# Kernel optimization log

Hardware: AMD Instinct MI355X
Metric: run time of the kernel (lower is better)

## Reference

```python
import jax, jax.numpy as jnp
import numpy as np

C = 768      # channel
H = 6        # height = 4 + 2*pre_step
W = 6        # width  = 4 + 2*pre_step
NB = 3       # n_block = H/2
SPLIT = 6    # = width
LS = 1536    # lstm_size = C * H / NB
NH = 4       # attention heads
DM = 512     # attention d_model
DK = DM // NH
B = 256


def setup_inputs() -> dict:
    key = jax.random.key(0)
    ks = jax.random.split(key, 20)
    s_l = 1.0 / np.sqrt(LS)
    s_a = 1.0 / np.sqrt(C)
    s_o = 1.0 / np.sqrt(DM)
    u = lambda k, shape, s: jax.random.uniform(k, shape, jnp.float32, -s, s)
    return {
        "x": jax.random.normal(ks[0], (B, H * W, C), jnp.float32),
        # 2-layer LSTM encoder (input=hidden=LS), torch gate order i,f,g,o
        "enc_Wih": u(ks[1], (2, 4 * LS, LS), s_l),
        "enc_Whh": u(ks[2], (2, 4 * LS, LS), s_l),
        "enc_bih": u(ks[3], (2, 4 * LS), s_l),
        "enc_bhh": u(ks[4], (2, 4 * LS), s_l),
        # 2-layer LSTM decoder
        "dec_Wih": u(ks[5], (2, 4 * LS, LS), s_l),
        "dec_Whh": u(ks[6], (2, 4 * LS, LS), s_l),
        "dec_bih": u(ks[7], (2, 4 * LS), s_l),
        "dec_bhh": u(ks[8], (2, 4 * LS), s_l),
        # multi-head attention: 768 -> 512 (4 heads x 128) -> 768
        "Wq": u(ks[9], (C, DM), s_a), "bq": u(ks[10], (DM,), s_a),
        "Wk": u(ks[11], (C, DM), s_a), "bk": u(ks[12], (DM,), s_a),
        "Wv": u(ks[13], (C, DM), s_a), "bv": u(ks[14], (DM,), s_a),
        "Wo": u(ks[15], (DM, C), s_o), "bo": u(ks[16], (C,), s_o),
        # LayerNorm over channel
        "ln_g": jnp.ones((C,), jnp.float32),
        "ln_b": jnp.zeros((C,), jnp.float32),
    }


def _cell(x, h, c, Wi, Wh, bi, bh):
    g = x @ Wi.T + bi + h @ Wh.T + bh
    i, f, gg, o = jnp.split(g, 4, axis=-1)
    c = jax.nn.sigmoid(f) * c + jax.nn.sigmoid(i) * jnp.tanh(gg)
    h = jax.nn.sigmoid(o) * jnp.tanh(c)
    return h, c


def _step2(st, xt, Wih, Whh, bih, bhh):
    # one timestep of a 2-layer LSTM
    h0, c0, h1, c1 = st
    h0, c0 = _cell(xt, h0, c0, Wih[0], Whh[0], bih[0], bhh[0])
    h1, c1 = _cell(h0, h1, c1, Wih[1], Whh[1], bih[1], bhh[1])
    return (h0, c0, h1, c1), h1


def _forward(x, enc_Wih, enc_Whh, enc_bih, enc_bhh,
             dec_Wih, dec_Whh, dec_bih, dec_bhh,
             Wq, bq, Wk, bk, Wv, bv, Wo, bo, ln_g, ln_b):
    Bx = x.shape[0]
    xb = x.reshape(Bx, NB, 2, W, C)
    # per block, each column j is a single-timestep feature concatenating the 2 rows
    # -> time-major sequence (SPLIT, NB*Bx, LS), blocks folded into the batch dim
    seq = jnp.transpose(xb, (3, 1, 0, 2, 4)).reshape(W, NB * Bx, LS)
    z = jnp.zeros((NB * Bx, LS), x.dtype)
    carry0 = (z, z, z, z)
    # encoder consumes columns in reversed order (j = split-1 .. 0)
    enc_st, enc_ys = jax.lax.scan(
        lambda s, xt: _step2(s, xt, enc_Wih, enc_Whh, enc_bih, enc_bhh),
        carry0, seq[::-1])
    en_out = enc_ys[-1]

    def dec_step(carry, _):
        st, inp = carry
        st, out = _step2(st, inp, dec_Wih, dec_Whh, dec_bih, dec_bhh)
        return (st, out), out
    _, dec_ys = jax.lax.scan(dec_step, (enc_st, en_out), None, length=SPLIT)

    # dec_ys: (SPLIT, NB*Bx, LS) -> xout_total: (NB, Bx, 2, SPLIT, C)
    xout = dec_ys.reshape(SPLIT, NB, Bx, 2, C).transpose(1, 2, 3, 0, 4)
    xt = xout.reshape(NB, Bx, 2 * SPLIT, C)

    # neighbor-block q/k, own-block v (NB=3): i=0 -> (q1,k2,v0); i=1 -> (q0,k2,v1); i=2 -> (q1,k0,v2)
    q = xt[jnp.array([1, 0, 1])]
    k = xt[jnp.array([2, 2, 0])]
    v = xt
    T = 2 * SPLIT
    Q = (q @ Wq + bq).reshape(NB, Bx, T, NH, DK)
    K = (k @ Wk + bk).reshape(NB, Bx, T, NH, DK)
    V = (v @ Wv + bv).reshape(NB, Bx, T, NH, DK)
    scores = jnp.einsum('nbqhd,nbkhd->nbhqk', Q, K) / np.float32(np.sqrt(DK))
    att = jax.nn.softmax(scores, axis=-1)
    o = jnp.einsum('nbhqk,nbkhd->nbqhd', att, V).reshape(NB, Bx, T, DM)
    o = o @ Wo + bo  # (NB, Bx, T, C)

    # concat blocks along height, layernorm over channel
    feat = o.reshape(NB, Bx, 2, W, C).transpose(1, 0, 2, 3, 4).reshape(Bx, H * W, C)
    mu = feat.mean(-1, keepdims=True)
    var = feat.var(-1, keepdims=True)
    feature = (feat - mu) / jnp.sqrt(var + 1e-5) * ln_g + ln_b
    out_decode = feature.reshape(Bx, H, W, C)[:, 1:5, 1:5, :]
    return feature, out_decode


def reference(x, enc_Wih, enc_Whh, enc_bih, enc_bhh,
              dec_Wih, dec_Whh, dec_bih, dec_bhh,
              Wq, bq, Wk, bk, Wv, bv, Wo, bo, ln_g, ln_b):
    return _forward(x, enc_Wih, enc_Whh, enc_bih, enc_bhh,
                    dec_Wih, dec_Whh, dec_bih, dec_bhh,
                    Wq, bq, Wk, bk, Wv, bv, Wo, bo, ln_g, ln_b)
```

## Files before the change

kernel.cpp:

```cpp
#include <hip/hip_runtime.h>


typedef unsigned short u16;
typedef unsigned int   u32;
typedef __bf16 bf16x8 __attribute__((ext_vector_type(8)));
typedef short  short8 __attribute__((ext_vector_type(8)));
typedef float  f32x4  __attribute__((ext_vector_type(4)));

__device__ __forceinline__ u16 f2bf(float f) {
  u32 u = __float_as_uint(f);
  u32 r = u + 0x7FFFu + ((u >> 16) & 1u);
  return (u16)(r >> 16);
}

__device__ __forceinline__ f32x4 mfma16(short8 a, short8 b, f32x4 c) {
  return __builtin_amdgcn_mfma_f32_16x16x32_bf16(
      __builtin_bit_cast(bf16x8, a), __builtin_bit_cast(bf16x8, b), c, 0, 0, 0);
}

__device__ __forceinline__ void gload16(const u16* g, u16* l) {
  __builtin_amdgcn_global_load_lds(
      (const __attribute__((address_space(1))) u32*)g,
      (__attribute__((address_space(3))) u32*)l, 16, 0, 0);
}

__global__ __launch_bounds__(256, 2) void lstm_cell(
    const u16* __restrict__ X, const u16* __restrict__ H,
    const u16* __restrict__ Wih, const u16* __restrict__ Whh,
    const float* __restrict__ bi, const float* __restrict__ bh,
    float* __restrict__ c, u16* __restrict__ hout, u16* __restrict__ h2)
{
  __shared__ __align__(16) u16 smem[32768];
  const int tid  = threadIdx.x;
  const int wid  = (blockIdx.x & 7) * 36 + (blockIdx.x >> 3);
  const int strip = wid / 6;
  const int bm    = wid - strip * 6;
  const int strip32 = strip * 32;
  const int lane = tid & 63, wave = tid >> 6;
  const int rh = wave & 1, hh = wave >> 1;
  const int r16  = lane & 15, kg = lane >> 4;
  const int srow = lane >> 2, sslot = lane & 3;

  f32x4 acc[4][4];
#pragma unroll
  for (int i = 0; i < 4; ++i)
#pragma unroll
    for (int j = 0; j < 4; ++j) acc[i][j] = (f32x4)0.0f;

  auto stage = [&](int i, int buf) {
    const u16* A = (i < 48) ? X : H;
    const u16* W = (i < 48) ? Wih : Whh;
    const int k0 = ((i < 48) ? i : (i - 48)) << 5;
#pragma unroll
    for (int cc2 = 0; cc2 < 2; ++cc2) {
      const int call = wave * 2 + cc2;
      const int row  = call * 16 + srow;
      const int slog = sslot ^ ((row >> 1) & 3);
      gload16(A + (size_t)(bm * 128 + row) * 1536 + k0 + slog * 8,
              smem + buf * 4096 + call * 512);
      const int g  = call >> 1;
      const int hr = (call & 1) * 16 + srow;
      gload16(W + ((size_t)g * 1536 + strip32 + hr) * 1536 + k0 + slog * 8,
              smem + 16384 + buf * 4096 + call * 512);
    }
  };

  auto computeFrom = [&](int i) {
    const u16* baseA = smem + (i & 3) * 4096;
    const u16* baseB = smem + 16384 + (i & 3) * 4096;
    short8 af[4], bfr[4];
#pragma unroll
    for (int mi = 0; mi < 4; ++mi) {
      const int row = rh * 64 + mi * 16 + r16;
      af[mi] = *(const short8*)(baseA + row * 32 + ((kg ^ ((row >> 1) & 3)) << 3));
    }
#pragma unroll
    for (int ni = 0; ni < 4; ++ni) {
      const int row = ni * 32 + hh * 16 + r16;
      bfr[ni] = *(const short8*)(baseB + row * 32 + ((kg ^ ((row >> 1) & 3)) << 3));
    }
#pragma unroll
    for (int mi = 0; mi < 4; ++mi)
#pragma unroll
      for (int ni = 0; ni < 4; ++ni)
        acc[mi][ni] = mfma16(af[mi], bfr[ni], acc[mi][ni]);
  };

  stage(0, 0); stage(1, 1); stage(2, 2); stage(3, 3);

  for (int i = 0; i < 93; ++i) {
    asm volatile("s_waitcnt vmcnt(12)" ::: "memory");
    __builtin_amdgcn_sched_barrier(0);
    __builtin_amdgcn_s_barrier();
    computeFrom(i);
    __builtin_amdgcn_s_barrier();
    __builtin_amdgcn_sched_barrier(0);
    if (i + 4 < 96) stage(i + 4, i & 3);
  }
  asm volatile("s_waitcnt vmcnt(8)" ::: "memory");
  __builtin_amdgcn_s_barrier();
  computeFrom(93);
  __builtin_amdgcn_s_barrier();
  asm volatile("s_waitcnt vmcnt(4)" ::: "memory");
  __builtin_amdgcn_s_barrier();
  computeFrom(94);
  __builtin_amdgcn_s_barrier();
  asm volatile("s_waitcnt vmcnt(0)" ::: "memory");
  __builtin_amdgcn_s_barrier();
  computeFrom(95);

  const int h = strip32 + hh * 16 + r16;
  float bsum[4];
#pragma unroll
  for (int ni = 0; ni < 4; ++ni)
    bsum[ni] = bi[ni * 1536 + h] + bh[ni * 1536 + h];
#pragma unroll
  for (int mi = 0; mi < 4; ++mi) {
    const int row0 = bm * 128 + rh * 64 + mi * 16 + kg * 4;
#pragma unroll
    for (int j = 0; j < 4; ++j) {
      const float ig = acc[mi][0][j] + bsum[0];
      const float fg = acc[mi][1][j] + bsum[1];
      const float gz = acc[mi][2][j] + bsum[2];
      const float og = acc[mi][3][j] + bsum[3];
      const float si = 1.0f / (1.0f + expf(-ig));
      const float sf = 1.0f / (1.0f + expf(-fg));
      const float so = 1.0f / (1.0f + expf(-og));
      const size_t cij = (size_t)(row0 + j) * 1536 + h;
      const float cnew = sf * c[cij] + si * tanhf(gz);
      c[cij] = cnew;
      const u16 hv = f2bf(so * tanhf(cnew));
      hout[cij] = hv;
      if (h2) h2[cij] = hv;
    }
  }
}

template <int OUT_BF16, int HAS_BIAS>
__global__ __launch_bounds__(256, 2) void gemm_bt(
    const u16* __restrict__ A1, const u16* __restrict__ B1, int K1,
    const float* __restrict__ bias, void* __restrict__ Cout, int N)
{
  __shared__ __align__(16) u16 smem[16384];
  const int tid  = threadIdx.x;
  const int bn   = blockIdx.x * 128;
  const int bm   = blockIdx.y * 128;
  const int lane = tid & 63, wave = tid >> 6;
  const int wm   = (wave >> 1) * 64, wn = (wave & 1) * 64;
  const int r16  = lane & 15, kg = lane >> 4;
  const int srow = lane >> 2, sslot = lane & 3;

  f32x4 acc[4][4];
#pragma unroll
  for (int i = 0; i < 4; ++i)
#pragma unroll
    for (int j = 0; j < 4; ++j) acc[i][j] = (f32x4)0.0f;

  const int nt = K1 >> 5;
  auto stage = [&](int i, int buf) {
    const int k0 = i << 5;
#pragma unroll
    for (int cc2 = 0; cc2 < 2; ++cc2) {
      const int call = wave * 2 + cc2;
      const int row  = call * 16 + srow;
      const int slog = sslot ^ ((row >> 1) & 3);
      gload16(A1 + (size_t)(bm + row) * K1 + k0 + slog * 8, smem + buf * 4096 + call * 512);
      gload16(B1 + (size_t)(bn + row) * K1 + k0 + slog * 8, smem + 8192 + buf * 4096 + call * 512);
    }
  };

  stage(0, 0);
  __syncthreads();
  int cur = 0;
  for (int i = 0; i < nt; ++i) {
    if (i + 1 < nt) stage(i + 1, cur ^ 1);
    const u16* baseA = smem + cur * 4096;
    const u16* baseB = smem + 8192 + cur * 4096;
    short8 af[4], bfr[4];
#pragma unroll
    for (int mi = 0; mi < 4; ++mi) {
      const int row = wm + mi * 16 + r16;
      af[mi] = *(const short8*)(baseA + row * 32 + ((kg ^ ((row >> 1) & 3)) << 3));
    }
#pragma unroll
    for (int ni = 0; ni < 4; ++ni) {
      const int row = wn + ni * 16 + r16;
      bfr[ni] = *(const short8*)(baseB + row * 32 + ((kg ^ ((row >> 1) & 3)) << 3));
    }
#pragma unroll
    for (int mi = 0; mi < 4; ++mi)
#pragma unroll
      for (int ni = 0; ni < 4; ++ni)
        acc[mi][ni] = mfma16(af[mi], bfr[ni], acc[mi][ni]);
    __syncthreads();
    cur ^= 1;
  }

  const size_t Ns = (size_t)N;
#pragma unroll
  for (int ni = 0; ni < 4; ++ni) {
    const int col = bn + wn + ni * 16 + r16;
    const float bvv = HAS_BIAS ? bias[col] : 0.0f;
#pragma unroll
    for (int mi = 0; mi < 4; ++mi) {
      const int row0 = bm + wm + mi * 16 + kg * 4;
      f32x4 v = acc[mi][ni];
#pragma unroll
      for (int j = 0; j < 4; ++j) {
        const float val = v[j] + bvv;
        const size_t idx = (size_t)(row0 + j) * Ns + col;
        if (OUT_BF16) ((u16*)Cout)[idx] = f2bf(val);
        else          ((float*)Cout)[idx] = val;
      }
    }
  }
}

__global__ __launch_bounds__(256) void attn_kernel(const u16* __restrict__ P, u16* __restrict__ O)
{
  __shared__ __align__(16) u16 sQ[12 * 520];
  __shared__ __align__(16) u16 sK[12 * 520];
  __shared__ __align__(16) u16 sVT[512 * 24];
  __shared__ __align__(16) u16 sS[4 * 16 * 16];
  const int tid = threadIdx.x;
  const int nb = blockIdx.x >> 8;
  const int b  = blockIdx.x & 255;
  const int qb = (nb == 1) ? 0 : 1;
  const int kb = (nb == 2) ? 0 : 2;
  const size_t rq = ((size_t)qb * 256 + b) * 12;
  const size_t rk = ((size_t)kb * 256 + b) * 12;
  const size_t rv = ((size_t)nb * 256 + b) * 12;

  for (int e4 = tid; e4 < 1536; e4 += 256) {
    const int t  = e4 >> 7;
    const int cc = (e4 & 127) * 4;
    uint2 qv = *(const uint2*)(P + (rq + t) * 1536 + cc);
    *(uint2*)(sQ + t * 520 + cc) = qv;
    uint2 kv = *(const uint2*)(P + (rk + t) * 1536 + 512 + cc);
    *(uint2*)(sK + t * 520 + cc) = kv;
    uint2 vv = *(const uint2*)(P + (rv + t) * 1536 + 1024 + cc);
    sVT[(cc + 0) * 24 + t] = (u16)(vv.x & 0xffff);
    sVT[(cc + 1) * 24 + t] = (u16)(vv.x >> 16);
    sVT[(cc + 2) * 24 + t] = (u16)(vv.y & 0xffff);
    sVT[(cc + 3) * 24 + t] = (u16)(vv.y >> 16);
  }
  for (int i = tid; i < 2048; i += 256) sVT[(i >> 2) * 24 + 12 + (i & 3)] = 0;
  __syncthreads();

  const int lane = tid & 63, h = tid >> 6;
  const int r16 = lane & 15, kg = lane >> 4;
  const int hcol = h * 128;

  f32x4 sc = (f32x4)0.0f;
#pragma unroll
  for (int ks = 0; ks < 4; ++ks) {
    short8 aq  = (r16 < 12) ? *(const short8*)(sQ + r16 * 520 + hcol + ks * 32 + kg * 8) : (short8)0;
    short8 bk2 = (r16 < 12) ? *(const short8*)(sK + r16 * 520 + hcol + ks * 32 + kg * 8) : (short8)0;
    sc = mfma16(aq, bk2, sc);
  }
  const float scale = 0.08838834764831845f;
#pragma unroll
  for (int j = 0; j < 4; ++j) {
    float v = (r16 < 12) ? sc[j] * scale : -1e30f;
    float m = v;
#pragma unroll
    for (int d = 1; d < 16; d <<= 1) m = fmaxf(m, __shfl_xor(m, d));
    float e = expf(v - m);
    float s = e;
#pragma unroll
    for (int d = 1; d < 16; d <<= 1) s += __shfl_xor(s, d);
    sS[h * 256 + (kg * 4 + j) * 16 + r16] = f2bf(e / s);
  }
  __syncthreads();
  short8 av = (kg < 2) ? *(const short8*)(sS + h * 256 + r16 * 16 + kg * 8) : (short8)0;
#pragma unroll
  for (int dt = 0; dt < 8; ++dt) {
    short8 bv2 = (kg < 2) ? *(const short8*)(sVT + (hcol + dt * 16 + r16) * 24 + kg * 8) : (short8)0;
    f32x4 ov = mfma16(av, bv2, (f32x4)0.0f);
    if (kg < 3) {
#pragma unroll
      for (int j = 0; j < 4; ++j) {
        const int q = kg * 4 + j;
        O[(rv + q) * 512 + hcol + dt * 16 + r16] = f2bf(ov[j]);
      }
    }
  }
}

__global__ __launch_bounds__(256) void layernorm_kernel(
    const float* __restrict__ feat, const float* __restrict__ gam,
    const float* __restrict__ bet, float* __restrict__ out)
{
  const int row = blockIdx.x;
  const int b = row / 36, hidx = row - b * 36;
  const int nb = hidx / 12, t = hidx - nb * 12;
  const float* src = feat + ((size_t)nb * 3072 + b * 12 + t) * 768;
  const int tid = threadIdx.x;
  float v0 = src[tid], v1 = src[tid + 256], v2 = src[tid + 512];
  float s = v0 + v1 + v2, sq = v0 * v0 + v1 * v1 + v2 * v2;
#pragma unroll
  for (int d = 1; d < 64; d <<= 1) { s += __shfl_xor(s, d); sq += __shfl_xor(sq, d); }
  __shared__ float ps[4], pq[4];
  if ((tid & 63) == 0) { ps[tid >> 6] = s; pq[tid >> 6] = sq; }
  __syncthreads();
  s  = ps[0] + ps[1] + ps[2] + ps[3];
  sq = pq[0] + pq[1] + pq[2] + pq[3];
  const float mean = s * (1.0f / 768.0f);
  const float var  = sq * (1.0f / 768.0f) - mean * mean;
  const float rstd = rsqrtf(var + 1e-5f);
  float* dst = out + (size_t)row * 768;
  const int hh = hidx / 6, wp = hidx - hh * 6;
  float* dst2 = nullptr;
  if (hh >= 1 && hh < 5 && wp >= 1 && wp < 5)
    dst2 = out + 7077888 + ((size_t)b * 16 + (hh - 1) * 4 + (wp - 1)) * 768;
#pragma unroll
  for (int i = 0; i < 3; ++i) {
    const int cix = tid + i * 256;
    const float vv = (i == 0) ? v0 : (i == 1 ? v1 : v2);
    const float o = (vv - mean) * rstd * gam[cix] + bet[cix];
    dst[cix] = o;
    if (dst2) dst2[cix] = o;
  }
}

__global__ __launch_bounds__(256) void cast_bf16_kernel(const float* __restrict__ src,
                                                        u16* __restrict__ dst, int n4)
{
  const int i = blockIdx.x * 256 + threadIdx.x;
  if (i >= n4) return;
  float4 v = ((const float4*)src)[i];
  uint2 pk;
  pk.x = (u32)f2bf(v.x) | ((u32)f2bf(v.y) << 16);
  pk.y = (u32)f2bf(v.z) | ((u32)f2bf(v.w) << 16);
  ((uint2*)dst)[i] = pk;
}

__global__ __launch_bounds__(256) void pack_qkvT(const float* __restrict__ Wq,
    const float* __restrict__ Wk, const float* __restrict__ Wv, u16* __restrict__ dst)
{
  const int idx = blockIdx.x * 256 + threadIdx.x;
  if (idx >= 1536 * 768) return;
  const int d = idx / 768, c = idx - d * 768;
  float v;
  if (d < 512)       v = Wq[(size_t)c * 512 + d];
  else if (d < 1024) v = Wk[(size_t)c * 512 + d - 512];
  else               v = Wv[(size_t)c * 512 + d - 1024];
  dst[idx] = f2bf(v);
}

__global__ __launch_bounds__(256) void pack_bias(const float* __restrict__ bq,
    const float* __restrict__ bk, const float* __restrict__ bv, float* __restrict__ dst)
{
  const int i = blockIdx.x * 256 + threadIdx.x;
  if (i < 512)       dst[i] = bq[i];
  else if (i < 1024) dst[i] = bk[i - 512];
  else if (i < 1536) dst[i] = bv[i - 1024];
}

__global__ __launch_bounds__(256) void pack_WoT(const float* __restrict__ Wo, u16* __restrict__ dst)
{
  const int idx = blockIdx.x * 256 + threadIdx.x;
  if (idx >= 768 * 512) return;
  const int n = idx / 512, k = idx - n * 512;
  dst[idx] = f2bf(Wo[(size_t)k * 768 + n]);
}

__global__ __launch_bounds__(256) void build_Xe(const float* __restrict__ x, u16* __restrict__ Xe)
{
  const int i4 = blockIdx.x * 256 + threadIdx.x;
  if (i4 >= 1769472) return;
  const int e = i4 * 4;
  const int c = e % 768;
  const int r2 = (e / 768) & 1;
  const int r = (e / 1536) % 768;
  const int s = e / 1179648;
  const int nb = r >> 8, bb = r & 255;
  const int w = 5 - s;
  const float* src = x + ((size_t)bb * 36 + (nb * 2 + r2) * 6 + w) * 768 + c;
  float4 v = *(const float4*)src;
  uint2 pk;
  pk.x = (u32)f2bf(v.x) | ((u32)f2bf(v.y) << 16);
  pk.y = (u32)f2bf(v.z) | ((u32)f2bf(v.w) << 16);
  ((uint2*)Xe)[i4] = pk;
}

__global__ __launch_bounds__(256) void build_xt(const u16* __restrict__ decys, u16* __restrict__ xt)
{
  const int i4 = blockIdx.x * 256 + threadIdx.x;
  if (i4 >= 1769472) return;
  const int e = i4 * 4;
  const int c = e % 768;
  const int t = (e / 768) % 12;
  const int b = (e / 9216) % 256;
  const int nb = e / 2359296;
  const int r2 = t / 6, s = t - r2 * 6;
  const u16* src = decys + ((size_t)s * 768 + nb * 256 + b) * 1536 + r2 * 768 + c;
  ((uint2*)xt)[i4] = *(const uint2*)src;
}

extern "C" void kernel_launch(void* const* d_in, const int* in_sizes, int n_in,
                              void* d_out, int out_size, void* d_ws, size_t ws_size,
                              hipStream_t stream)
{
  const float* x    = (const float*)d_in[0];
  const float* eWih = (const float*)d_in[1];
  const float* eWhh = (const float*)d_in[2];
  const float* ebih = (const float*)d_in[3];
  const float* ebhh = (const float*)d_in[4];
  const float* dWih = (const float*)d_in[5];
  const float* dWhh = (const float*)d_in[6];
  const float* dbih = (const float*)d_in[7];
  const float* dbhh = (const float*)d_in[8];
  const float* Wq = (const float*)d_in[9];
  const float* bq = (const float*)d_in[10];
  const float* Wk = (const float*)d_in[11];
  const float* bk = (const float*)d_in[12];
  const float* Wv = (const float*)d_in[13];
  const float* bv = (const float*)d_in[14];
  const float* Wo = (const float*)d_in[15];
  const float* bo = (const float*)d_in[16];
  const float* lng = (const float*)d_in[17];
  const float* lnb = (const float*)d_in[18];

  char* ws = (char*)d_ws;
  const size_t WBYTES = 37748736;
  u16* Weih = (u16*)(ws);
  u16* Wehh = (u16*)(ws + WBYTES);
  u16* Wdih = (u16*)(ws + 2 * WBYTES);
  u16* Wdhh = (u16*)(ws + 3 * WBYTES);
  u16*   xtb   = (u16*)(ws);
  u16*   Pqkv  = (u16*)(ws + 14155776);
  u16*   Obuf  = (u16*)(ws + 14155776 + 28311552);
  float* feato = (float*)(ws + 14155776 + 28311552 + 9437184);
  size_t off = 4 * WBYTES;
  auto take = [&](size_t bytes) -> char* {
    char* p = ws + off;
    off = (off + bytes + 255) & ~(size_t)255;
    return p;
  };
  u16* Wqkv  = (u16*)take((size_t)1536 * 768 * 2);
  float* bqkv = (float*)take(1536 * 4);
  u16* WoT   = (u16*)take((size_t)768 * 512 * 2);
  u16* Xe    = (u16*)take((size_t)6 * 768 * 1536 * 2);
  u16* h0a   = (u16*)take((size_t)768 * 1536 * 2);
  u16* h0b   = (u16*)take((size_t)768 * 1536 * 2);
  u16* h1a   = (u16*)take((size_t)768 * 1536 * 2);
  u16* h1b   = (u16*)take((size_t)768 * 1536 * 2);
  float* c0  = (float*)take((size_t)768 * 1536 * 4);
  float* c1  = (float*)take((size_t)768 * 1536 * 4);
  u16* decys = (u16*)take((size_t)6 * 768 * 1536 * 2);
  if (off > ws_size) return;

  const size_t WL = (size_t)6144 * 1536;
  const dim3 blk(256);

  cast_bf16_kernel<<<18432, blk, 0, stream>>>(eWih, Weih, 4718592);
  cast_bf16_kernel<<<18432, blk, 0, stream>>>(eWhh, Wehh, 4718592);
  cast_bf16_kernel<<<18432, blk, 0, stream>>>(dWih, Wdih, 4718592);
  cast_bf16_kernel<<<18432, blk, 0, stream>>>(dWhh, Wdhh, 4718592);
  pack_qkvT<<<4608, blk, 0, stream>>>(Wq, Wk, Wv, Wqkv);
  pack_bias<<<6, blk, 0, stream>>>(bq, bk, bv, bqkv);
  pack_WoT<<<1536, blk, 0, stream>>>(Wo, WoT);
  build_Xe<<<6912, blk, 0, stream>>>(x, Xe);

  hipMemsetAsync(h0a, 0, (size_t)768 * 1536 * 2, stream);
  hipMemsetAsync(h1a, 0, (size_t)768 * 1536 * 2, stream);
  hipMemsetAsync(c0, 0, (size_t)768 * 1536 * 4, stream);
  hipMemsetAsync(c1, 0, (size_t)768 * 1536 * 4, stream);

  u16* h0[2] = {h0a, h0b};
  u16* h1[2] = {h1a, h1b};
  int p = 0;
  for (int s = 0; s < 6; ++s) {
    lstm_cell<<<288, blk, 0, stream>>>(Xe + (size_t)s * 768 * 1536, h0[p],
                                       Weih, Wehh, ebih, ebhh, c0, h0[p ^ 1], nullptr);
    lstm_cell<<<288, blk, 0, stream>>>(h0[p ^ 1], h1[p],
                                       Weih + WL, Wehh + WL, ebih + 6144, ebhh + 6144,
                                       c1, h1[p ^ 1], nullptr);
    p ^= 1;
  }
  for (int t = 0; t < 6; ++t) {
    lstm_cell<<<288, blk, 0, stream>>>(h1[p], h0[p],
                                       Wdih, Wdhh, dbih, dbhh, c0, h0[p ^ 1], nullptr);
    lstm_cell<<<288, blk, 0, stream>>>(h0[p ^ 1], h1[p],
                                       Wdih + WL, Wdhh + WL, dbih + 6144, dbhh + 6144,
                                       c1, h1[p ^ 1], decys + (size_t)t * 768 * 1536);
    p ^= 1;
  }
  build_xt<<<6912, blk, 0, stream>>>(decys, xtb);
  gemm_bt<1, 1><<<dim3(12, 72), blk, 0, stream>>>(xtb, Wqkv, 768, bqkv, Pqkv, 1536);
  attn_kernel<<<768, blk, 0, stream>>>(Pqkv, Obuf);
  gemm_bt<0, 1><<<dim3(6, 72), blk, 0, stream>>>(Obuf, WoT, 512, bo, feato, 768);
  layernorm_kernel<<<9216, blk, 0, stream>>>(feato, lng, lnb, (float*)d_out);
}
```

Baseline: 1.321 ms.

## Deepen LSTM GEMM LDS ring to six stages and halve barriers per k-step

The LDS staging ring in the LSTM cell GEMM grows from four to six buffers. The main loop now consumes two k-slices per iteration with a single workgroup barrier, and issues the next two prefetches before computing instead of after. This is meant to cut barrier and waitcnt overhead and keep more global loads in flight. The cost is larger shared memory per block (96KB) and the loss of the two-blocks-per-CU launch bound, which likely lowers occupancy.

```diff
diff --git a/kernel.cpp b/kernel.cpp
--- a/kernel.cpp
+++ b/kernel.cpp
@@ -24,13 +24,13 @@
       (__attribute__((address_space(3))) u32*)l, 16, 0, 0);
 }
 
-__global__ __launch_bounds__(256, 2) void lstm_cell(
+__global__ __launch_bounds__(256) void lstm_cell(
     const u16* __restrict__ X, const u16* __restrict__ H,
     const u16* __restrict__ Wih, const u16* __restrict__ Whh,
     const float* __restrict__ bi, const float* __restrict__ bh,
     float* __restrict__ c, u16* __restrict__ hout, u16* __restrict__ h2)
 {
-  __shared__ __align__(16) u16 smem[32768];
+  __shared__ __align__(16) u16 smem[49152];
   const int tid  = threadIdx.x;
   const int wid  = (blockIdx.x & 7) * 36 + (blockIdx.x >> 3);
   const int strip = wid / 6;
@@ -47,10 +47,11 @@
 #pragma unroll
     for (int j = 0; j < 4; ++j) acc[i][j] = (f32x4)0.0f;
 
-  auto stage = [&](int i, int buf) {
-    const u16* A = (i < 48) ? X : H;
-    const u16* W = (i < 48) ? Wih : Whh;
-    const int k0 = ((i < 48) ? i : (i - 48)) << 5;
+  auto stage = [&](int s) {
+    const int buf = s % 6;
+    const u16* A = (s < 48) ? X : H;
+    const u16* W = (s < 48) ? Wih : Whh;
+    const int k0 = ((s < 48) ? s : (s - 48)) << 5;
 #pragma unroll
     for (int cc2 = 0; cc2 < 2; ++cc2) {
       const int call = wave * 2 + cc2;
@@ -61,13 +62,13 @@
       const int g  = call >> 1;
       const int hr = (call & 1) * 16 + srow;
       gload16(W + ((size_t)g * 1536 + strip32 + hr) * 1536 + k0 + slog * 8,
-              smem + 16384 + buf * 4096 + call * 512);
+              smem + 24576 + buf * 4096 + call * 512);
     }
   };
 
-  auto computeFrom = [&](int i) {
-    const u16* baseA = smem + (i & 3) * 4096;
-    const u16* baseB = smem + 16384 + (i & 3) * 4096;
+  auto computeFrom = [&](int s) {
+    const u16* baseA = smem + (s % 6) * 4096;
+    const u16* baseB = smem + 24576 + (s % 6) * 4096;
     short8 af[4], bfr[4];
 #pragma unroll
     for (int mi = 0; mi < 4; ++mi) {
@@ -86,27 +87,23 @@
         acc[mi][ni] = mfma16(af[mi], bfr[ni], acc[mi][ni]);
   };
 
-  stage(0, 0); stage(1, 1); stage(2, 2); stage(3, 3);
-
-  for (int i = 0; i < 93; ++i) {
-    asm volatile("s_waitcnt vmcnt(12)" ::: "memory");
+  stage(0); stage(1); stage(2); stage(3);
+
+  for (int p = 0; p < 47; ++p) {
+    asm volatile("s_waitcnt vmcnt(8)" ::: "memory");
     __builtin_amdgcn_sched_barrier(0);
     __builtin_amdgcn_s_barrier();
-    computeFrom(i);
-    __builtin_amdgcn_s_barrier();
+    const int s0 = 2 * p + 4, s1 = 2 * p + 5;
+    if (s0 < 96) stage(s0);
+    if (s1 < 96) stage(s1);
+    computeFrom(2 * p);
+    computeFrom(2 * p + 1);
     __builtin_amdgcn_sched_barrier(0);
-    if (i + 4 < 96) stage(i + 4, i & 3);
-  }
-  asm volatile("s_waitcnt vmcnt(8)" ::: "memory");
-  __builtin_amdgcn_s_barrier();
-  computeFrom(93);
-  __builtin_amdgcn_s_barrier();
-  asm volatile("s_waitcnt vmcnt(4)" ::: "memory");
+  }
+  asm volatile("s_waitcnt vmcnt(0)" ::: "memory");
+  __builtin_amdgcn_sched_barrier(0);
   __builtin_amdgcn_s_barrier();
   computeFrom(94);
-  __builtin_amdgcn_s_barrier();
-  asm volatile("s_waitcnt vmcnt(0)" ::: "memory");
-  __builtin_amdgcn_s_barrier();
   computeFrom(95);
 
   const int h = strip32 + hh * 16 + r16;
```

Result: slower. 2.545 ms (+92.6%).
